# Kernel optimization log

Measured on AMD Instinct MI355X. Metric: run time of the kernel, lower is better.

The kernel has to match this reference:

```python
import jax, jax.numpy as jnp
import numpy as np

CONF_THRES = 0.25   # NMS.conf
IOU_THRES = 0.45    # NMS.iou
MAX_NMS = 1024      # fixed candidate count so greedy NMS is jit-compatible
IMG = 640.0


def setup_inputs() -> dict:
    key = jax.random.key(0)
    k0, k1, k2, k3, k4 = jax.random.split(key, 5)
    B, N = 32, 25200
    cxcy = jax.random.uniform(k0, (B, N, 2), dtype=jnp.float32) * IMG
    wh = jax.random.uniform(k1, (B, N, 2), dtype=jnp.float32) * 80.0 + 2.0
    obj = jax.random.uniform(k2, (B, N, 1), dtype=jnp.float32)
    lmk = jax.random.uniform(k3, (B, N, 10), dtype=jnp.float32) * IMG
    cls = jax.random.uniform(k4, (B, N, 1), dtype=jnp.float32)
    # layout: [cx, cy, w, h, obj, 10 landmark coords, 1 class score]
    prediction = jnp.concatenate([cxcy, wh, obj, lmk, cls], axis=2)
    return {"prediction": prediction}


def xywh2xyxy(x):
    cx, cy, w, h = x[:, 0], x[:, 1], x[:, 2], x[:, 3]
    return jnp.stack([cx - w / 2, cy - h / 2, cx + w / 2, cy + h / 2], axis=1)


def pairwise_iou(b):  # b: [K,4] xyxy -> [K,K]
    area = (b[:, 2] - b[:, 0]) * (b[:, 3] - b[:, 1])
    lt = jnp.maximum(b[:, None, :2], b[None, :, :2])
    rb = jnp.minimum(b[:, None, 2:], b[None, :, 2:])
    wh = jnp.clip(rb - lt, 0.0)
    inter = wh[..., 0] * wh[..., 1]
    return inter / (area[:, None] + area[None, :] - inter + 1e-7)


def _nms_image(pred):  # pred: [N,16]
    obj = pred[:, 4]
    score = pred[:, 15] * obj  # x[:,15:] *= x[:,4:5]; nc==1 -> single class, j==0
    valid = (obj > CONF_THRES) & (score > CONF_THRES)  # xc filter + conf filter
    s = jnp.where(valid, score, -1.0)
    top_s, idx = jax.lax.top_k(s, MAX_NMS)  # score-sorted candidates (greedy NMS order)
    x = pred[idx]  # [K,16]
    box = xywh2xyxy(x[:, :4])
    vmask = top_s > 0.0  # valid candidates (invalid slots carry score -1)
    # class offset c = j*4096 is identically 0 since nc==1 -> skip
    iou = pairwise_iou(box)  # [K,K]
    rng = jnp.arange(MAX_NMS)

    def step(keep, i):
        sup = keep[i] & (iou[i] > IOU_THRES) & (rng > i)
        return keep & ~sup, None

    keep, _ = jax.lax.scan(step, vmask, rng)
    det = jnp.concatenate(
        [box, top_s[:, None], x[:, 5:15], jnp.zeros((MAX_NMS, 1), pred.dtype)], axis=1
    )  # [K,16] = box(4) | conf(1) | landmarks(10) | class(1)=0
    return det * keep[:, None].astype(det.dtype), keep


def reference(prediction):
    # Fixed-shape analogue of the per-image ragged output: detections padded to
    # MAX_NMS rows per image (zeroed where suppressed) plus a keep mask.
    det, keep = jax.vmap(_nms_image)(prediction)
    return det, keep
```

## Files before the change

kernel.cpp:

```cpp
#include <hip/hip_runtime.h>
#include <stdint.h>

#define NB 32
#define NN 25200
#define NN4 6300
#define TOPK 1024
#define NF 16
#define CONF 0.25f
#define IOU_T 0.45f
#define NBIN 4096
#define CAP 2048
#define KEY_BASE 0xBE800001u

__device__ __forceinline__ uint32_t score_key(float obj, float cls) {
  float score = __fmul_rn(cls, obj);
  bool valid = (obj > CONF) && (score > CONF);
  float s = valid ? score : -1.0f;
  uint32_t u = __float_as_uint(s);
  return (u & 0x80000000u) ? ~u : (u | 0x80000000u);
}

__device__ __forceinline__ uint64_t shfl_xor_u64(uint64_t v, int m) {
  uint32_t lo = __shfl_xor((uint32_t)v, m, 64);
  uint32_t hi = __shfl_xor((uint32_t)(v >> 32), m, 64);
  return ((uint64_t)hi << 32) | lo;
}

__global__ void k_keys(const float* __restrict__ pred, uint32_t* __restrict__ keys) {
  int g = blockIdx.x * blockDim.x + threadIdx.x;
  if (g >= NB * NN) return;
  const float* row = pred + (size_t)g * NF;
  keys[g] = score_key(row[4], row[15]);
}

__global__ __launch_bounds__(1024) void k_select(const uint32_t* __restrict__ keys,
                                                 int* __restrict__ sel) {
  int b = blockIdx.x;
  int tid = threadIdx.x;
  int lane = tid & 63, wid = tid >> 6;
  const uint32_t* kb = keys + (size_t)b * NN;
  const uint4* kb4 = (const uint4*)kb;
  __shared__ uint32_t hist[NBIN];
  __shared__ uint64_t ent[CAP];
  __shared__ uint32_t wsum[16];
  __shared__ uint32_t sh_bin;
  __shared__ uint32_t sh_cnt;
  #pragma unroll
  for (int k = 0; k < 4; ++k) hist[tid + 1024 * k] = 0;
  ent[tid] = 0; ent[tid + 1024] = 0;
  if (tid == 0) { sh_cnt = 0; sh_bin = 0; }
  __syncthreads();

  for (int i = tid; i < NN4; i += 1024) {
    uint4 k4 = kb4[i];
    uint32_t kv[4] = {k4.x, k4.y, k4.z, k4.w};
    #pragma unroll
    for (int c = 0; c < 4; ++c) {
      uint32_t key = kv[c];
      if (key >= KEY_BASE) {
        uint32_t bin = (key - KEY_BASE) >> 12;
        if (bin > NBIN - 1) bin = NBIN - 1;
        atomicAdd(&hist[bin], 1u);
      }
    }
  }
  __syncthreads();

  uint32_t h[4]; uint32_t s = 0;
  #pragma unroll
  for (int k = 0; k < 4; ++k) { h[k] = hist[NBIN - 1 - (4 * tid + k)]; s += h[k]; }
  uint32_t my = s;
  #pragma unroll
  for (int d = 1; d < 64; d <<= 1) {
    uint32_t v = __shfl_up(s, d, 64);
    if (lane >= d) s += v;
  }
  if (lane == 63) wsum[wid] = s;
  __syncthreads();
  uint32_t base = 0;
  for (int w = 0; w < wid; ++w) base += wsum[w];
  uint32_t cum = base + s - my;
  #pragma unroll
  for (int k = 0; k < 4; ++k) {
    if (cum < TOPK && cum + h[k] >= TOPK) sh_bin = (uint32_t)(NBIN - 1 - (4 * tid + k));
    cum += h[k];
  }
  __syncthreads();
  uint32_t thr = KEY_BASE + (sh_bin << 12);

  for (int i = tid; i < NN4; i += 1024) {
    uint4 k4 = kb4[i];
    uint32_t kv[4] = {k4.x, k4.y, k4.z, k4.w};
    #pragma unroll
    for (int c = 0; c < 4; ++c) {
      uint32_t key = kv[c];
      if (key >= thr) {
        uint32_t p = atomicAdd(&sh_cnt, 1u);
        if (p < CAP) ent[p] = ((uint64_t)key << 32) | (uint32_t)(~(uint32_t)(4 * i + c));
      }
    }
  }
  __syncthreads();

  uint64_t v0 = ent[tid], v1 = ent[tid + 1024];
  for (unsigned kk = 2; kk <= CAP; kk <<= 1) {
    for (unsigned j = kk >> 1; j > 0; j >>= 1) {
      if (j == 1024) {
        uint64_t mx = v0 > v1 ? v0 : v1;
        uint64_t mn = v0 > v1 ? v1 : v0;
        v0 = mx; v1 = mn;
      } else if (j >= 64) {
        __syncthreads();
        ent[tid] = v0; ent[tid + 1024] = v1;
        __syncthreads();
        uint64_t p0 = ent[tid ^ j], p1 = ent[(tid ^ j) + 1024];
        bool low = ((tid & j) == 0);
        bool d0 = ((tid & kk) == 0);
        bool d1 = (((tid + 1024) & kk) == 0);
        v0 = (low != d0) ? (v0 < p0 ? v0 : p0) : (v0 > p0 ? v0 : p0);
        v1 = (low != d1) ? (v1 < p1 ? v1 : p1) : (v1 > p1 ? v1 : p1);
      } else {
        uint64_t p0 = shfl_xor_u64(v0, (int)j);
        uint64_t p1 = shfl_xor_u64(v1, (int)j);
        bool low = ((tid & j) == 0);
        bool d0 = ((tid & kk) == 0);
        bool d1 = (((tid + 1024) & kk) == 0);
        v0 = (low != d0) ? (v0 < p0 ? v0 : p0) : (v0 > p0 ? v0 : p0);
        v1 = (low != d1) ? (v1 < p1 ? v1 : p1) : (v1 > p1 ? v1 : p1);
      }
    }
  }
  uint32_t n = ~(uint32_t)(v0 & 0xFFFFFFFFu);
  if (n >= NN) n = 0;
  sel[(size_t)b * TOPK + tid] = (int)n;
}

__global__ __launch_bounds__(1024) void k_mask(const float* __restrict__ pred,
                                               const int* __restrict__ sel,
                                               uint32_t* __restrict__ mask) {
  int b = blockIdx.x;
  int sblk = blockIdx.y;
  int tid = threadIdx.x;
  int rg = tid & 31;
  int cc = tid >> 5;
  __shared__ float bx1[TOPK], by1[TOPK], bx2[TOPK], by2[TOPK], bar[TOPK];
  {
    int n = sel[(size_t)b * TOPK + tid];
    const float4* row = (const float4*)(pred + ((size_t)b * NN + n) * NF);
    float4 r0 = row[0];
    float hw = __fmul_rn(r0.z, 0.5f), hh = __fmul_rn(r0.w, 0.5f);
    float x1 = __fsub_rn(r0.x, hw), y1 = __fsub_rn(r0.y, hh);
    float x2 = __fadd_rn(r0.x, hw), y2 = __fadd_rn(r0.y, hh);
    bx1[tid] = x1; by1[tid] = y1; bx2[tid] = x2; by2[tid] = y2;
    bar[tid] = __fmul_rn(__fsub_rn(x2, x1), __fsub_rn(y2, y1));
  }
  __syncthreads();
  int i0 = sblk * 128 + rg * 4;
  int iw = i0 >> 5;
  uint32_t wreg[4] = {0u, 0u, 0u, 0u};
  if (cc >= iw) {
    float rx1[4], ry1[4], rx2[4], ry2[4], rar[4];
    #pragma unroll
    for (int k = 0; k < 4; ++k) {
      rx1[k] = bx1[i0 + k]; ry1[k] = by1[i0 + k];
      rx2[k] = bx2[i0 + k]; ry2[k] = by2[i0 + k]; rar[k] = bar[i0 + k];
    }
    for (int jj = 0; jj < 32; ++jj) {
      int j = cc * 32 + jj;
      float cx1 = bx1[j], cy1 = by1[j], cx2 = bx2[j], cy2 = by2[j], car = bar[j];
      #pragma unroll
      for (int k = 0; k < 4; ++k) {
        float lx = fmaxf(rx1[k], cx1);
        float ly = fmaxf(ry1[k], cy1);
        float rx = fminf(rx2[k], cx2);
        float ry = fminf(ry2[k], cy2);
        float wd = fmaxf(__fsub_rn(rx, lx), 0.0f);
        float ht = fmaxf(__fsub_rn(ry, ly), 0.0f);
        float inter = __fmul_rn(wd, ht);
        float den = __fadd_rn(__fsub_rn(__fadd_rn(rar[k], car), inter), 1e-7f);
        float iou = __fdiv_rn(inter, den);
        wreg[k] |= (iou > IOU_T ? 1u : 0u) << jj;
      }
    }
    if (cc == iw) {
      #pragma unroll
      for (int k = 0; k < 4; ++k)
        wreg[k] &= ~((2u << ((i0 + k) & 31)) - 1u);
    }
  }
  uint4 out = make_uint4(wreg[0], wreg[1], wreg[2], wreg[3]);
  *(uint4*)&mask[((size_t)b * 32 + cc) * TOPK + i0] = out;
}

__global__ __launch_bounds__(1024, 4) void k_scan_out(const float* __restrict__ pred,
                                                      const int* __restrict__ sel,
                                                      const uint32_t* __restrict__ mask,
                                                      float* __restrict__ det,
                                                      float* __restrict__ keep_out) {
  int b = blockIdx.x;
  int tid = threadIdx.x;
  int lane = tid & 63, wv = tid >> 6;
  __shared__ uint32_t vbits[32];
  __shared__ uint32_t keepw[32];

  int n = sel[(size_t)b * TOPK + tid];
  const float4* rowv = (const float4*)(pred + ((size_t)b * NN + n) * NF);
  float4 r0 = rowv[0], r1 = rowv[1], r2 = rowv[2], r3 = rowv[3];
  float obj = r1.x, cls = r3.w;
  float score = __fmul_rn(cls, obj);
  bool valid = (obj > CONF) && (score > CONF);
  uint64_t bal = __ballot(valid);
  if (lane == 0) {
    vbits[2 * wv] = (uint32_t)bal;
    vbits[2 * wv + 1] = (uint32_t)(bal >> 32);
  }
  __syncthreads();

  if (tid < 32) {
    int l = tid;
    uint32_t kw = vbits[l];
    const uint4* mc = (const uint4*)(mask + (size_t)b * (32 * TOPK) + (size_t)l * TOPK);
    uint32_t cur[32], nxt[32];
    #pragma unroll
    for (int q = 0; q < 8; ++q) *(uint4*)&cur[4 * q] = mc[q];
    for (int w = 0; w < 32; ++w) {
      if (w < 31) {
        #pragma unroll
        for (int q = 0; q < 8; ++q) *(uint4*)&nxt[4 * q] = mc[(w + 1) * 8 + q];
      }
      uint32_t rw = kw;
      #pragma unroll
      for (int t = 0; t < 32; ++t)
        if ((rw >> t) & 1u) rw &= ~cur[t];
      uint32_t rf = __shfl(rw, w, 64);
      if (l == w) {
        kw = rf;
      } else if (l > w) {
        uint32_t acc = 0;
        #pragma unroll
        for (int t = 0; t < 32; ++t) acc |= ((rf >> t) & 1u) ? cur[t] : 0u;
        kw &= ~acc;
      }
      if (w < 31) {
        #pragma unroll
        for (int t = 0; t < 32; ++t) cur[t] = nxt[t];
      }
    }
    keepw[l] = kw;
  }
  __syncthreads();

  bool kept = (keepw[tid >> 5] >> (tid & 31)) & 1u;
  float m = kept ? 1.0f : 0.0f;
  float hw = __fmul_rn(r0.z, 0.5f), hh = __fmul_rn(r0.w, 0.5f);
  float4 o0 = make_float4(__fsub_rn(r0.x, hw) * m, __fsub_rn(r0.y, hh) * m,
                          __fadd_rn(r0.x, hw) * m, __fadd_rn(r0.y, hh) * m);
  float4 o1 = make_float4(score * m, r1.y * m, r1.z * m, r1.w * m);
  float4 o2 = make_float4(r2.x * m, r2.y * m, r2.z * m, r2.w * m);
  float4 o3 = make_float4(r3.x * m, r3.y * m, r3.z * m, 0.0f);
  float4* dst = (float4*)(det + ((size_t)b * TOPK + tid) * NF);
  dst[0] = o0; dst[1] = o1; dst[2] = o2; dst[3] = o3;
  keep_out[(size_t)b * TOPK + tid] = m;
}

extern "C" void kernel_launch(void* const* d_in, const int* in_sizes, int n_in,
                              void* d_out, int out_size, void* d_ws, size_t ws_size,
                              hipStream_t stream) {
  const float* pred = (const float*)d_in[0];
  float* det = (float*)d_out;
  float* keep = det + (size_t)NB * TOPK * NF;

  uint8_t* ws = (uint8_t*)d_ws;
  uint32_t* keys = (uint32_t*)ws;
  int* sel = (int*)(ws + (size_t)NB * NN * 4);
  uint32_t* mask = (uint32_t*)(ws + (size_t)NB * NN * 4
                                  + (size_t)NB * TOPK * 4);

  k_keys<<<(NB * NN + 255) / 256, 256, 0, stream>>>(pred, keys);
  k_select<<<NB, 1024, 0, stream>>>(keys, sel);
  dim3 gm(NB, 8);
  k_mask<<<gm, 1024, 0, stream>>>(pred, sel, mask);
  k_scan_out<<<NB, 1024, 0, stream>>>(pred, sel, mask, det, keep);
}
```

Before: 167.6 us.

## Fuse key computation into select and merge mask with scan via last-block counter

Folds the separate key-generation kernel into the per-image selection kernel: keys are computed straight from the prediction rows and cached in a 100KB LDS array for the second pass, so the global key buffer round trip is gone. The mask and scan/output kernels are merged, and the last of the 8 mask blocks per image, found through an atomic counter with release/acquire fences, performs the greedy scan and writes the output. Launches drop from four to two. In exchange, the selection kernel now reads strided 16-float rows with only 32 blocks, which may cost load bandwidth, and its large LDS footprint limits occupancy. The scan also moves into a kernel without the earlier occupancy launch bound, so it may get fewer registers.

```diff
diff --git a/kernel.cpp b/kernel.cpp
--- a/kernel.cpp
+++ b/kernel.cpp
@@ -3,7 +3,6 @@
 
 #define NB 32
 #define NN 25200
-#define NN4 6300
 #define TOPK 1024
 #define NF 16
 #define CONF 0.25f
@@ -26,20 +25,14 @@
   return ((uint64_t)hi << 32) | lo;
 }
 
-__global__ void k_keys(const float* __restrict__ pred, uint32_t* __restrict__ keys) {
-  int g = blockIdx.x * blockDim.x + threadIdx.x;
-  if (g >= NB * NN) return;
-  const float* row = pred + (size_t)g * NF;
-  keys[g] = score_key(row[4], row[15]);
-}
-
-__global__ __launch_bounds__(1024) void k_select(const uint32_t* __restrict__ keys,
-                                                 int* __restrict__ sel) {
+__global__ __launch_bounds__(1024) void k_sel(const float* __restrict__ pred,
+                                              int* __restrict__ sel,
+                                              uint32_t* __restrict__ cnt) {
   int b = blockIdx.x;
   int tid = threadIdx.x;
   int lane = tid & 63, wid = tid >> 6;
-  const uint32_t* kb = keys + (size_t)b * NN;
-  const uint4* kb4 = (const uint4*)kb;
+  const float* pb = pred + (size_t)b * NN * NF;
+  __shared__ uint32_t lkeys[NN];
   __shared__ uint32_t hist[NBIN];
   __shared__ uint64_t ent[CAP];
   __shared__ uint32_t wsum[16];
@@ -48,20 +41,18 @@
   #pragma unroll
   for (int k = 0; k < 4; ++k) hist[tid + 1024 * k] = 0;
   ent[tid] = 0; ent[tid + 1024] = 0;
-  if (tid == 0) { sh_cnt = 0; sh_bin = 0; }
-  __syncthreads();
-
-  for (int i = tid; i < NN4; i += 1024) {
-    uint4 k4 = kb4[i];
-    uint32_t kv[4] = {k4.x, k4.y, k4.z, k4.w};
-    #pragma unroll
-    for (int c = 0; c < 4; ++c) {
-      uint32_t key = kv[c];
-      if (key >= KEY_BASE) {
-        uint32_t bin = (key - KEY_BASE) >> 12;
-        if (bin > NBIN - 1) bin = NBIN - 1;
-        atomicAdd(&hist[bin], 1u);
-      }
+  if (tid == 0) { sh_cnt = 0; sh_bin = 0; cnt[b] = 0; }
+  __syncthreads();
+
+  for (int n = tid; n < NN; n += 1024) {
+    float obj = pb[(size_t)n * NF + 4];
+    float cls = pb[(size_t)n * NF + 15];
+    uint32_t key = score_key(obj, cls);
+    lkeys[n] = key;
+    if (key >= KEY_BASE) {
+      uint32_t bin = (key - KEY_BASE) >> 12;
+      if (bin > NBIN - 1) bin = NBIN - 1;
+      atomicAdd(&hist[bin], 1u);
     }
   }
   __syncthreads();
@@ -88,16 +79,11 @@
   __syncthreads();
   uint32_t thr = KEY_BASE + (sh_bin << 12);
 
-  for (int i = tid; i < NN4; i += 1024) {
-    uint4 k4 = kb4[i];
-    uint32_t kv[4] = {k4.x, k4.y, k4.z, k4.w};
-    #pragma unroll
-    for (int c = 0; c < 4; ++c) {
-      uint32_t key = kv[c];
-      if (key >= thr) {
-        uint32_t p = atomicAdd(&sh_cnt, 1u);
-        if (p < CAP) ent[p] = ((uint64_t)key << 32) | (uint32_t)(~(uint32_t)(4 * i + c));
-      }
+  for (int n = tid; n < NN; n += 1024) {
+    uint32_t key = lkeys[n];
+    if (key >= thr) {
+      uint32_t p = atomicAdd(&sh_cnt, 1u);
+      if (p < CAP) ent[p] = ((uint64_t)key << 32) | (uint32_t)(~(uint32_t)n);
     }
   }
   __syncthreads();
@@ -135,17 +121,24 @@
   sel[(size_t)b * TOPK + tid] = (int)n;
 }
 
-__global__ __launch_bounds__(1024) void k_mask(const float* __restrict__ pred,
-                                               const int* __restrict__ sel,
-                                               uint32_t* __restrict__ mask) {
+__global__ __launch_bounds__(1024) void k_mask_scan(const float* __restrict__ pred,
+                                                    const int* __restrict__ sel,
+                                                    uint32_t* __restrict__ mask,
+                                                    uint32_t* __restrict__ cnt,
+                                                    float* __restrict__ det,
+                                                    float* __restrict__ keep_out) {
   int b = blockIdx.x;
   int sblk = blockIdx.y;
   int tid = threadIdx.x;
   int rg = tid & 31;
   int cc = tid >> 5;
   __shared__ float bx1[TOPK], by1[TOPK], bx2[TOPK], by2[TOPK], bar[TOPK];
+  __shared__ uint32_t sh_old;
+  __shared__ uint32_t vbits[32];
+  __shared__ uint32_t keepw[32];
+
+  int n = sel[(size_t)b * TOPK + tid];
   {
-    int n = sel[(size_t)b * TOPK + tid];
     const float4* row = (const float4*)(pred + ((size_t)b * NN + n) * NF);
     float4 r0 = row[0];
     float hw = __fmul_rn(r0.z, 0.5f), hh = __fmul_rn(r0.w, 0.5f);
@@ -155,6 +148,7 @@
     bar[tid] = __fmul_rn(__fsub_rn(x2, x1), __fsub_rn(y2, y1));
   }
   __syncthreads();
+
   int i0 = sblk * 128 + rg * 4;
   int iw = i0 >> 5;
   uint32_t wreg[4] = {0u, 0u, 0u, 0u};
@@ -188,22 +182,20 @@
         wreg[k] &= ~((2u << ((i0 + k) & 31)) - 1u);
     }
   }
-  uint4 out = make_uint4(wreg[0], wreg[1], wreg[2], wreg[3]);
-  *(uint4*)&mask[((size_t)b * 32 + cc) * TOPK + i0] = out;
-}
-
-__global__ __launch_bounds__(1024, 4) void k_scan_out(const float* __restrict__ pred,
-                                                      const int* __restrict__ sel,
-                                                      const uint32_t* __restrict__ mask,
-                                                      float* __restrict__ det,
-                                                      float* __restrict__ keep_out) {
-  int b = blockIdx.x;
-  int tid = threadIdx.x;
+  *(uint4*)&mask[((size_t)b * 32 + cc) * TOPK + i0] =
+      make_uint4(wreg[0], wreg[1], wreg[2], wreg[3]);
+  __syncthreads();
+
+  if (tid == 0) {
+    __builtin_amdgcn_fence(__ATOMIC_RELEASE, "agent");
+    sh_old = __hip_atomic_fetch_add(&cnt[b], 1u, __ATOMIC_ACQ_REL,
+                                    __HIP_MEMORY_SCOPE_AGENT);
+  }
+  __syncthreads();
+  if (sh_old != 7) return;
+  __builtin_amdgcn_fence(__ATOMIC_ACQUIRE, "agent");
+
   int lane = tid & 63, wv = tid >> 6;
-  __shared__ uint32_t vbits[32];
-  __shared__ uint32_t keepw[32];
-
-  int n = sel[(size_t)b * TOPK + tid];
   const float4* rowv = (const float4*)(pred + ((size_t)b * NN + n) * NF);
   float4 r0 = rowv[0], r1 = rowv[1], r2 = rowv[2], r3 = rowv[3];
   float obj = r1.x, cls = r3.w;
@@ -271,14 +263,12 @@
   float* keep = det + (size_t)NB * TOPK * NF;
 
   uint8_t* ws = (uint8_t*)d_ws;
-  uint32_t* keys = (uint32_t*)ws;
-  int* sel = (int*)(ws + (size_t)NB * NN * 4);
-  uint32_t* mask = (uint32_t*)(ws + (size_t)NB * NN * 4
-                                  + (size_t)NB * TOPK * 4);
-
-  k_keys<<<(NB * NN + 255) / 256, 256, 0, stream>>>(pred, keys);
-  k_select<<<NB, 1024, 0, stream>>>(keys, sel);
+  int* sel = (int*)ws;
+  uint32_t* mask = (uint32_t*)(ws + (size_t)NB * TOPK * 4);
+  uint32_t* cnt = (uint32_t*)(ws + (size_t)NB * TOPK * 4
+                                 + (size_t)NB * 32 * TOPK * 4);
+
+  k_sel<<<NB, 1024, 0, stream>>>(pred, sel, cnt);
   dim3 gm(NB, 8);
-  k_mask<<<gm, 1024, 0, stream>>>(pred, sel, mask);
-  k_scan_out<<<NB, 1024, 0, stream>>>(pred, sel, mask, det, keep);
-}
+  k_mask_scan<<<gm, 1024, 0, stream>>>(pred, sel, mask, cnt, det, keep);
+}
```

Measured after the change: 194.7 us. +16.2%, slower.
